# Kernel tuning notes

Measured on AMD Instinct MI355X. Metric: run time of the kernel, lower is better.

The kernel has to match this reference:

```python
import jax, jax.numpy as jnp
import numpy as np


def setup_inputs() -> dict:
    key = jax.random.key(0)
    ks = jax.random.split(key, 5)
    B, N, L, d = 8, 2048, 2048, 512
    q = N // 4
    return {
        "logits": jax.random.normal(ks[0], (B, N, L), jnp.float32),
        "emb0": jax.random.normal(ks[1], (q, d), jnp.float32),
        "emb1": jax.random.normal(ks[2], (q, d), jnp.float32),
        "emb2": jax.random.normal(ks[3], (q, d), jnp.float32),
        "emb3": jax.random.normal(ks[4], (q, d), jnp.float32),
    }


def reference(logits, emb0, emb1, emb2, emb3):
    # Eval / late-epoch path of Embedding.forward (process_block_max, k=3):
    # per head: top-k over codebook dim -> masked softmax -> einsum combine.
    # softmax over only the top-k values is mathematically identical to
    # softmax of the -inf-masked full logits, and gathering the k codebook
    # rows is identical to the dense einsum 'bnl,nm->bml' with that sparse attn.
    K = 3
    B, N, L = logits.shape
    E = jnp.stack([emb0, emb1, emb2, emb3])            # (4, q, d)
    q = E.shape[1]
    lg = logits.reshape(B, 4, q, L).transpose(0, 1, 3, 2)  # (B, 4, L, q)
    vals, idx = jax.lax.top_k(lg, K)                   # (B, 4, L, K)
    w = jax.nn.softmax(vals, axis=-1)                  # sparse attn weights

    def head(emb_h, idx_h, w_h):
        g = emb_h[idx_h]                               # (B, L, K, d) gather
        return jnp.einsum('blk,blkd->bld', w_h, g)     # (B, L, d)

    outs = jax.vmap(head, in_axes=(0, 1, 1))(E, idx, w)  # (4, B, L, d)
    # output = out_0 + out_1 + out_2 + out_3, returned as (B, d, L)
    return outs.sum(axis=0).transpose(0, 2, 1)
```

## Files before the change

kernel.cpp:

```cpp
#include <hip/hip_runtime.h>
#include <math.h>

#define BB 8
#define NN 2048
#define LL 2048
#define QQ 512
#define DD 512

__global__ __launch_bounds__(256) void topk_kernel(
    const float* __restrict__ logits, float4* __restrict__ wpack) {
  const int u  = threadIdx.x & 63;
  const int g  = threadIdx.x >> 6;
  const int lt = blockIdx.x;
  const int h  = blockIdx.y;
  const int b  = blockIdx.z;
  const int l4 = lt * 256 + u * 4;

  const float* base =
      logits + ((size_t)(b * NN + h * QQ + g * 128) * LL) + l4;

  float v0[4], v1[4], v2[4];
  int   i0[4], i1[4], i2[4];
#pragma unroll
  for (int j = 0; j < 4; ++j) {
    v0[j] = v1[j] = v2[j] = -INFINITY;
    i0[j] = i1[j] = i2[j] = 0;
  }

#pragma unroll 8
  for (int n = 0; n < 128; ++n) {
    const float4 vv = *(const float4*)(base + (size_t)n * LL);
    const int i = g * 128 + n;
    const float ve[4] = {vv.x, vv.y, vv.z, vv.w};
#pragma unroll
    for (int j = 0; j < 4; ++j) {
      float v = ve[j];
      bool gt0 = v > v0[j], gt1 = v > v1[j], gt2 = v > v2[j];
      float nv2 = gt1 ? v1[j] : (gt2 ? v : v2[j]);
      int   ni2 = gt1 ? i1[j] : (gt2 ? i : i2[j]);
      float nv1 = gt0 ? v0[j] : (gt1 ? v : v1[j]);
      int   ni1 = gt0 ? i0[j] : (gt1 ? i : i1[j]);
      v0[j] = gt0 ? v : v0[j];
      i0[j] = gt0 ? i : i0[j];
      v1[j] = nv1; i1[j] = ni1; v2[j] = nv2; i2[j] = ni2;
    }
  }

  __shared__ float sv[4][256][3];
  __shared__ int   si[4][256][3];
#pragma unroll
  for (int j = 0; j < 4; ++j) {
    const int ll = u * 4 + j;
    sv[g][ll][0] = v0[j]; sv[g][ll][1] = v1[j]; sv[g][ll][2] = v2[j];
    si[g][ll][0] = i0[j]; si[g][ll][1] = i1[j]; si[g][ll][2] = i2[j];
  }
  __syncthreads();

  const int t = threadIdx.x;
  float m0 = sv[0][t][0], m1 = sv[0][t][1], m2 = sv[0][t][2];
  int   j0 = si[0][t][0], j1 = si[0][t][1], j2 = si[0][t][2];
#pragma unroll
  for (int gg = 1; gg < 4; ++gg) {
#pragma unroll
    for (int k = 0; k < 3; ++k) {
      float v = sv[gg][t][k];
      int   i = si[gg][t][k];
      bool gt0 = v > m0, gt1 = v > m1, gt2 = v > m2;
      float nv2 = gt1 ? m1 : (gt2 ? v : m2);
      int   ni2 = gt1 ? j1 : (gt2 ? i : j2);
      float nv1 = gt0 ? m0 : (gt1 ? v : m1);
      int   ni1 = gt0 ? j0 : (gt1 ? i : j1);
      m0 = gt0 ? v : m0;
      j0 = gt0 ? i : j0;
      m1 = nv1; j1 = ni1; m2 = nv2; j2 = ni2;
    }
  }
  float e1 = __expf(m1 - m0), e2 = __expf(m2 - m0);
  float inv = 1.0f / (1.0f + e1 + e2);
  unsigned int pi = (unsigned int)j0 | ((unsigned int)j1 << 9) |
                    ((unsigned int)j2 << 18);
  float4 W = make_float4(inv, e1 * inv, e2 * inv, __uint_as_float(pi));
  wpack[(size_t)(b * 4 + h) * LL + lt * 256 + t] = W;
}

__global__ __launch_bounds__(256) void combine_kernel(
    const float4* __restrict__ wpack,
    const float* __restrict__ emb0, const float* __restrict__ emb1,
    const float* __restrict__ emb2, const float* __restrict__ emb3,
    float* __restrict__ out) {
  const int u    = threadIdx.x & 63;
  const int w    = threadIdx.x >> 6;
  const int lblk = blockIdx.x * 16;
  const int b    = blockIdx.y;

  __shared__ float tile[16][516];

  const float* embs[4] = {emb0, emb1, emb2, emb3};

#pragma unroll
  for (int il = 0; il < 4; ++il) {
    const int l = lblk + w * 4 + il;
    float wt[12];
    const float* rows[12];
#pragma unroll
    for (int h = 0; h < 4; ++h) {
      float4 W = wpack[(size_t)(b * 4 + h) * LL + l];
      unsigned int pi = __float_as_uint(W.w);
      wt[h * 3 + 0] = W.x;
      wt[h * 3 + 1] = W.y;
      wt[h * 3 + 2] = W.z;
      rows[h * 3 + 0] = embs[h] + (size_t)(pi & 511) * DD;
      rows[h * 3 + 1] = embs[h] + (size_t)((pi >> 9) & 511) * DD;
      rows[h * 3 + 2] = embs[h] + (size_t)((pi >> 18) & 511) * DD;
    }
#pragma unroll
    for (int p = 0; p < 2; ++p) {
      const int d = p * 256 + u * 4;
      float a0 = 0.f, a1 = 0.f, a2 = 0.f, a3 = 0.f;
#pragma unroll
      for (int m = 0; m < 12; ++m) {
        const float4 e = *(const float4*)(rows[m] + d);
        a0 += wt[m] * e.x;
        a1 += wt[m] * e.y;
        a2 += wt[m] * e.z;
        a3 += wt[m] * e.w;
      }
      float4 a = make_float4(a0, a1, a2, a3);
      *(float4*)&tile[w * 4 + il][d] = a;
    }
  }
  __syncthreads();

  const int l0  = (threadIdx.x & 3) * 4;
  const int dof = threadIdx.x >> 2;
  float* outb = out + (size_t)b * DD * LL + lblk + l0;
#pragma unroll
  for (int dd = 0; dd < 512; dd += 64) {
    const int d = dd + dof;
    float4 r;
    r.x = tile[l0 + 0][d];
    r.y = tile[l0 + 1][d];
    r.z = tile[l0 + 2][d];
    r.w = tile[l0 + 3][d];
    *(float4*)(outb + (size_t)d * LL) = r;
  }
}

extern "C" void kernel_launch(void* const* d_in, const int* in_sizes, int n_in,
                              void* d_out, int out_size, void* d_ws,
                              size_t ws_size, hipStream_t stream) {
  const float* logits = (const float*)d_in[0];
  const float* emb0   = (const float*)d_in[1];
  const float* emb1   = (const float*)d_in[2];
  const float* emb2   = (const float*)d_in[3];
  const float* emb3   = (const float*)d_in[4];
  float*       out    = (float*)d_out;
  float4*      wpack  = (float4*)d_ws;

  dim3 ga(LL / 256, 4, BB);
  topk_kernel<<<ga, 256, 0, stream>>>(logits, wpack);

  dim3 gb(LL / 16, BB);
  combine_kernel<<<gb, 256, 0, stream>>>(wpack, emb0, emb1, emb2, emb3, out);
}
```

Measured before the change: 253.5 us.

## Split top-k scan across four N-slices with a separate merge kernel

The top-k stage previously launched 256 blocks, each scanning 128 rows per wave group. It now splits the codebook dimension into four slices, launching 1024 blocks that each scan 32 rows per group, and batches eight float4 loads before the compare chain to expose memory-level parallelism. A new merge kernel combines the four partial top-3 results and computes the softmax weights. This is meant to raise occupancy and bandwidth use on the 128MB logits read. The cost is an extra launch and partial-result traffic through workspace.

```diff
diff --git a/kernel.cpp b/kernel.cpp
--- a/kernel.cpp
+++ b/kernel.cpp
@@ -7,17 +7,31 @@
 #define QQ 512
 #define DD 512
 
-__global__ __launch_bounds__(256) void topk_kernel(
-    const float* __restrict__ logits, float4* __restrict__ wpack) {
+__device__ __forceinline__ void top3_insert(float v, int i, float& m0,
+                                            float& m1, float& m2, int& j0,
+                                            int& j1, int& j2) {
+  bool gt0 = v > m0, gt1 = v > m1, gt2 = v > m2;
+  float nv2 = gt1 ? m1 : (gt2 ? v : m2);
+  int   ni2 = gt1 ? j1 : (gt2 ? i : j2);
+  float nv1 = gt0 ? m0 : (gt1 ? v : m1);
+  int   ni1 = gt0 ? j0 : (gt1 ? i : j1);
+  m0 = gt0 ? v : m0;
+  j0 = gt0 ? i : j0;
+  m1 = nv1; j1 = ni1; m2 = nv2; j2 = ni2;
+}
+
+__global__ __launch_bounds__(256) void topk_part_kernel(
+    const float* __restrict__ logits, float4* __restrict__ part) {
   const int u  = threadIdx.x & 63;
   const int g  = threadIdx.x >> 6;
   const int lt = blockIdx.x;
   const int h  = blockIdx.y;
-  const int b  = blockIdx.z;
+  const int b  = blockIdx.z >> 2;
+  const int ns = blockIdx.z & 3;
   const int l4 = lt * 256 + u * 4;
+  const int n0 = ns * 128 + g * 32;
 
-  const float* base =
-      logits + ((size_t)(b * NN + h * QQ + g * 128) * LL) + l4;
+  const float* base = logits + ((size_t)(b * NN + h * QQ + n0) * LL) + l4;
 
   float v0[4], v1[4], v2[4];
   int   i0[4], i1[4], i2[4];
@@ -27,22 +41,18 @@
     i0[j] = i1[j] = i2[j] = 0;
   }
 
-#pragma unroll 8
-  for (int n = 0; n < 128; ++n) {
-    const float4 vv = *(const float4*)(base + (size_t)n * LL);
-    const int i = g * 128 + n;
-    const float ve[4] = {vv.x, vv.y, vv.z, vv.w};
+  float4 buf[8];
+  for (int t = 0; t < 4; ++t) {
 #pragma unroll
-    for (int j = 0; j < 4; ++j) {
-      float v = ve[j];
-      bool gt0 = v > v0[j], gt1 = v > v1[j], gt2 = v > v2[j];
-      float nv2 = gt1 ? v1[j] : (gt2 ? v : v2[j]);
-      int   ni2 = gt1 ? i1[j] : (gt2 ? i : i2[j]);
-      float nv1 = gt0 ? v0[j] : (gt1 ? v : v1[j]);
-      int   ni1 = gt0 ? i0[j] : (gt1 ? i : i1[j]);
-      v0[j] = gt0 ? v : v0[j];
-      i0[j] = gt0 ? i : i0[j];
-      v1[j] = nv1; i1[j] = ni1; v2[j] = nv2; i2[j] = ni2;
+    for (int p = 0; p < 8; ++p)
+      buf[p] = *(const float4*)(base + (size_t)(t * 8 + p) * LL);
+#pragma unroll
+    for (int p = 0; p < 8; ++p) {
+      const int i = n0 + t * 8 + p;
+      top3_insert(buf[p].x, i, v0[0], v1[0], v2[0], i0[0], i1[0], i2[0]);
+      top3_insert(buf[p].y, i, v0[1], v1[1], v2[1], i0[1], i1[1], i2[1]);
+      top3_insert(buf[p].z, i, v0[2], v1[2], v2[2], i0[2], i1[2], i2[2]);
+      top3_insert(buf[p].w, i, v0[3], v1[3], v2[3], i0[3], i1[3], i2[3]);
     }
   }
 
@@ -60,27 +70,42 @@
   float m0 = sv[0][t][0], m1 = sv[0][t][1], m2 = sv[0][t][2];
   int   j0 = si[0][t][0], j1 = si[0][t][1], j2 = si[0][t][2];
 #pragma unroll
-  for (int gg = 1; gg < 4; ++gg) {
+  for (int gg = 1; gg < 4; ++gg)
 #pragma unroll
-    for (int k = 0; k < 3; ++k) {
-      float v = sv[gg][t][k];
-      int   i = si[gg][t][k];
-      bool gt0 = v > m0, gt1 = v > m1, gt2 = v > m2;
-      float nv2 = gt1 ? m1 : (gt2 ? v : m2);
-      int   ni2 = gt1 ? j1 : (gt2 ? i : j2);
-      float nv1 = gt0 ? m0 : (gt1 ? v : m1);
-      int   ni1 = gt0 ? j0 : (gt1 ? i : j1);
-      m0 = gt0 ? v : m0;
-      j0 = gt0 ? i : j0;
-      m1 = nv1; j1 = ni1; m2 = nv2; j2 = ni2;
-    }
+    for (int k = 0; k < 3; ++k)
+      top3_insert(sv[gg][t][k], si[gg][t][k], m0, m1, m2, j0, j1, j2);
+
+  unsigned int pi = (unsigned int)j0 | ((unsigned int)j1 << 9) |
+                    ((unsigned int)j2 << 18);
+  part[(size_t)(((b * 4 + h) * 4 + ns)) * LL + lt * 256 + t] =
+      make_float4(m0, m1, m2, __uint_as_float(pi));
+}
+
+__global__ __launch_bounds__(256) void topk_merge_kernel(
+    const float4* __restrict__ part, float4* __restrict__ wpack) {
+  const int x   = blockIdx.x;
+  const int bh  = x >> 3;
+  const int l   = (x & 7) * 256 + threadIdx.x;
+  const size_t base = (size_t)bh * 4 * LL + l;
+
+  float4 P = part[base];
+  float m0 = P.x, m1 = P.y, m2 = P.z;
+  unsigned int pi = __float_as_uint(P.w);
+  int j0 = pi & 511, j1 = (pi >> 9) & 511, j2 = (pi >> 18) & 511;
+#pragma unroll
+  for (int ns = 1; ns < 4; ++ns) {
+    float4 Q = part[base + (size_t)ns * LL];
+    unsigned int qi = __float_as_uint(Q.w);
+    top3_insert(Q.x, qi & 511, m0, m1, m2, j0, j1, j2);
+    top3_insert(Q.y, (qi >> 9) & 511, m0, m1, m2, j0, j1, j2);
+    top3_insert(Q.z, (qi >> 18) & 511, m0, m1, m2, j0, j1, j2);
   }
   float e1 = __expf(m1 - m0), e2 = __expf(m2 - m0);
   float inv = 1.0f / (1.0f + e1 + e2);
-  unsigned int pi = (unsigned int)j0 | ((unsigned int)j1 << 9) |
+  unsigned int po = (unsigned int)j0 | ((unsigned int)j1 << 9) |
                     ((unsigned int)j2 << 18);
-  float4 W = make_float4(inv, e1 * inv, e2 * inv, __uint_as_float(pi));
-  wpack[(size_t)(b * 4 + h) * LL + lt * 256 + t] = W;
+  wpack[(size_t)bh * LL + l] =
+      make_float4(inv, e1 * inv, e2 * inv, __uint_as_float(po));
 }
 
 __global__ __launch_bounds__(256) void combine_kernel(
@@ -125,8 +150,7 @@
         a2 += wt[m] * e.z;
         a3 += wt[m] * e.w;
       }
-      float4 a = make_float4(a0, a1, a2, a3);
-      *(float4*)&tile[w * 4 + il][d] = a;
+      *(float4*)&tile[w * 4 + il][d] = make_float4(a0, a1, a2, a3);
     }
   }
   __syncthreads();
@@ -155,10 +179,14 @@
   const float* emb2   = (const float*)d_in[3];
   const float* emb3   = (const float*)d_in[4];
   float*       out    = (float*)d_out;
-  float4*      wpack  = (float4*)d_ws;
 
-  dim3 ga(LL / 256, 4, BB);
-  topk_kernel<<<ga, 256, 0, stream>>>(logits, wpack);
+  float4* part  = (float4*)d_ws;
+  float4* wpack = (float4*)((char*)d_ws + (size_t)8 * 4 * 4 * LL * 16);
+
+  dim3 ga(8, 4, 32);
+  topk_part_kernel<<<ga, 256, 0, stream>>>(logits, part);
+
+  topk_merge_kernel<<<256, 256, 0, stream>>>(part, wpack);
 
   dim3 gb(LL / 16, BB);
   combine_kernel<<<gb, 256, 0, stream>>>(wpack, emb0, emb1, emb2, emb3, out);
```

New measurement: 234.2 us. -7.6%, faster.
